# Kernel tuning notes

Measured on AMD Instinct MI355X. Metric: run time of the kernel, lower is better.

Reference implementation:

```python
import jax, jax.numpy as jnp
import numpy as np

L, B, T, S, W, H = 4, 2, 2048, 512, 512, 8  # layers, batch, n_ctx, cond units, width, heads
CH = W // H


def _ln(x, g, b):
    m = x.mean(-1, keepdims=True)
    v = ((x - m) ** 2).mean(-1, keepdims=True)
    return (x - m) * jax.lax.rsqrt(v + 1e-5) * g + b


def setup_inputs() -> dict:
    key = jax.random.key(0)
    ks = jax.random.split(key, 16)
    std = 0.25 * np.sqrt(1.0 / W)  # init_scale * sqrt(1/width), as in Transformer.__init__
    f32 = jnp.float32
    d = {
        "x": jax.random.normal(ks[0], (B, T, W), f32),
        "cond_k": jax.random.normal(ks[1], (B, S, W), f32),
        "cond_v": jax.random.normal(ks[2], (B, S, W), f32),
        # stacked per-layer params; weights stored [in, out] (torch Linear transposed)
        "qkv_w": jax.random.normal(ks[3], (L, W, 3 * W), f32) * std,
        "qkv_b": jnp.zeros((L, 3 * W), f32),
        "attn_proj_w": jax.random.normal(ks[4], (L, W, W), f32) * std,
        "attn_proj_b": jnp.zeros((L, W), f32),
        "cross_proj_w": jax.random.normal(ks[5], (L, W, W), f32) * std,
        "cross_proj_b": jnp.zeros((L, W), f32),
        "fc_w": jax.random.normal(ks[6], (L, W, 4 * W), f32) * std,
        "fc_b": jnp.zeros((L, 4 * W), f32),
        "mlp_proj_w": jax.random.normal(ks[7], (L, 4 * W, W), f32) * std,
        "mlp_proj_b": jnp.zeros((L, W), f32),
        "ln1_g": jnp.ones((L, W), f32), "ln1_b": jnp.zeros((L, W), f32),
        "ln3_g": jnp.ones((L, W), f32), "ln3_b": jnp.zeros((L, W), f32),
        "ln4_g": jnp.ones((L, W), f32), "ln4_b": jnp.zeros((L, W), f32),
    }
    return d


def reference(x, cond_k, cond_v, qkv_w, qkv_b, attn_proj_w, attn_proj_b,
              cross_proj_w, cross_proj_b, fc_w, fc_b, mlp_proj_w, mlp_proj_b,
              ln1_g, ln1_b, ln3_g, ln3_b, ln4_g, ln4_b):
    b, t, w = x.shape
    ch = w // H
    scale = 1.0 / np.sqrt(np.sqrt(ch))  # applied to both q and k, as in torch code
    kk = cond_k.reshape(b, -1, H, ch)
    vv = cond_v.reshape(b, -1, H, ch)
    n_layers = qkv_w.shape[0]
    for i in range(n_layers):
        # ---- self-attention ----
        h = _ln(x, ln1_g[i], ln1_b[i])
        qkv = (h @ qkv_w[i] + qkv_b[i]).reshape(b, t, H, 3 * ch)
        q, k, v = qkv[..., :ch], qkv[..., ch:2 * ch], qkv[..., 2 * ch:]
        wts = jnp.einsum('bthc,bshc->bhts', q * scale, k * scale)
        wts = jax.nn.softmax(wts.astype(jnp.float32), axis=-1).astype(wts.dtype)
        a = jnp.einsum('bhts,bshc->bthc', wts, v).reshape(b, t, w)
        x = x + a @ attn_proj_w[i] + attn_proj_b[i]
        # ---- cross-attention (q is ln_3(x) directly, no q projection) ----
        h = _ln(x, ln3_g[i], ln3_b[i])
        q = h.reshape(b, t, H, ch)
        wts = jnp.einsum('bthc,bshc->bhts', q * scale, kk * scale)
        wts = jax.nn.softmax(wts.astype(jnp.float32), axis=-1).astype(wts.dtype)
        a = jnp.einsum('bhts,bshc->bthc', wts, vv).reshape(b, t, w)
        x = x + a @ cross_proj_w[i] + cross_proj_b[i]
        # ---- MLP (exact erf GELU, as torch nn.GELU default) ----
        h = _ln(x, ln4_g[i], ln4_b[i])
        h = jax.nn.gelu(h @ fc_w[i] + fc_b[i], approximate=False)
        x = x + h @ mlp_proj_w[i] + mlp_proj_b[i]
    return x
```

## Files before the change

kernel.cpp:

```cpp
#include <hip/hip_runtime.h>
#include <hip/hip_bf16.h>
#include <cstdint>


typedef __bf16 bf16;
typedef __bf16 bf16x8 __attribute__((ext_vector_type(8)));
typedef float f32x4 __attribute__((ext_vector_type(4)));

#define AS1(p) ((__attribute__((address_space(1))) void*)(uintptr_t)(p))
#define AS3(p) ((__attribute__((address_space(3))) void*)(p))

__device__ __forceinline__ unsigned short bf2us(bf16 v) {
    return __builtin_bit_cast(unsigned short, v);
}

__global__ __launch_bounds__(256) void ln_kernel(const float* __restrict__ x,
                                                 const float* __restrict__ gam,
                                                 const float* __restrict__ bet,
                                                 bf16* __restrict__ h) {
    int row  = blockIdx.x * 4 + (threadIdx.x >> 6);
    int lane = threadIdx.x & 63;
    const float4* xr = (const float4*)(x + (size_t)row * 512) + lane * 2;
    float4 a = xr[0], b = xr[1];
    float s  = a.x + a.y + a.z + a.w + b.x + b.y + b.z + b.w;
    float ss = a.x * a.x + a.y * a.y + a.z * a.z + a.w * a.w +
               b.x * b.x + b.y * b.y + b.z * b.z + b.w * b.w;
#pragma unroll
    for (int off = 1; off < 64; off <<= 1) {
        s  += __shfl_xor(s, off);
        ss += __shfl_xor(ss, off);
    }
    float mean = s * (1.f / 512.f);
    float var  = ss * (1.f / 512.f) - mean * mean;
    float rstd = rsqrtf(fmaxf(var, 0.f) + 1e-5f);
    const float4* gr = (const float4*)gam + lane * 2;
    const float4* br = (const float4*)bet + lane * 2;
    float4 g0 = gr[0], g1 = gr[1], b0 = br[0], b1 = br[1];
    bf16x8 hv;
    hv[0] = (bf16)((a.x - mean) * rstd * g0.x + b0.x);
    hv[1] = (bf16)((a.y - mean) * rstd * g0.y + b0.y);
    hv[2] = (bf16)((a.z - mean) * rstd * g0.z + b0.z);
    hv[3] = (bf16)((a.w - mean) * rstd * g0.w + b0.w);
    hv[4] = (bf16)((b.x - mean) * rstd * g1.x + b1.x);
    hv[5] = (bf16)((b.y - mean) * rstd * g1.y + b1.y);
    hv[6] = (bf16)((b.z - mean) * rstd * g1.z + b1.z);
    hv[7] = (bf16)((b.w - mean) * rstd * g1.w + b1.w);
    *(bf16x8*)(h + (size_t)row * 512 + lane * 8) = hv;
}

__global__ void wtrans_kernel(const float* __restrict__ in, bf16* __restrict__ out,
                              int K, int N) {
    __shared__ float tile[32][33];
    int n0 = blockIdx.x * 32, k0 = blockIdx.y * 32;
    const float* ip = in + (size_t)blockIdx.z * K * N;
    bf16* op = out + (size_t)blockIdx.z * N * K;
#pragma unroll
    for (int i = threadIdx.y; i < 32; i += 8)
        tile[i][threadIdx.x] = ip[(size_t)(k0 + i) * N + n0 + threadIdx.x];
    __syncthreads();
#pragma unroll
    for (int i = threadIdx.y; i < 32; i += 8)
        op[(size_t)(n0 + i) * K + k0 + threadIdx.x] = (bf16)tile[threadIdx.x][i];
}

__global__ void cvt_kernel(const float* __restrict__ in, bf16* __restrict__ out, int n) {
    int i = (blockIdx.x * 256 + threadIdx.x) * 8;
    if (i + 8 <= n) {
        const float4* p = (const float4*)(in + i);
        float4 a = p[0], b = p[1];
        bf16x8 v;
        v[0] = (bf16)a.x; v[1] = (bf16)a.y; v[2] = (bf16)a.z; v[3] = (bf16)a.w;
        v[4] = (bf16)b.x; v[5] = (bf16)b.y; v[6] = (bf16)b.z; v[7] = (bf16)b.w;
        *(bf16x8*)(out + i) = v;
    }
}

__global__ __launch_bounds__(256) void vtrans_self(const bf16* __restrict__ qkvb,
                                                   bf16* __restrict__ VTs, int T_) {
    __shared__ bf16 tl[64][66];
    int tb = blockIdx.x * 64;
    int bh = blockIdx.y;
    int b = bh >> 3, h = bh & 7;
    int tid = threadIdx.x;
#pragma unroll
    for (int e = 0; e < 2; ++e) {
        int idx = e * 256 + tid;
        int t = idx >> 3, ci = (idx & 7) * 8;
        bf16x8 v = *(const bf16x8*)(qkvb + ((size_t)b * T_ + tb + t) * 1536 +
                                    h * 192 + 128 + ci);
#pragma unroll
        for (int j = 0; j < 8; ++j) tl[ci + j][t] = v[j];
    }
    __syncthreads();
#pragma unroll
    for (int e = 0; e < 2; ++e) {
        int idx = e * 256 + tid;
        int ch = idx >> 3, ti = (idx & 7) * 8;
        bf16x8 v;
#pragma unroll
        for (int j = 0; j < 8; ++j) v[j] = tl[ch][ti + j];
        *(bf16x8*)(VTs + ((size_t)bh * 64 + ch) * T_ + tb + ti) = v;
    }
}

__global__ __launch_bounds__(256) void vtrans_cross(const float* __restrict__ cv,
                                                    bf16* __restrict__ VTc, int S_) {
    __shared__ bf16 tl[64][66];
    int sb = blockIdx.x * 64;
    int bh = blockIdx.y;
    int b = bh >> 3, h = bh & 7;
    int tid = threadIdx.x;
#pragma unroll
    for (int e = 0; e < 4; ++e) {
        int idx = e * 256 + tid;
        int s = idx >> 4, ci = (idx & 15) * 4;
        float4 v = *(const float4*)(cv + ((size_t)b * S_ + sb + s) * 512 + h * 64 + ci);
        tl[ci + 0][s] = (bf16)v.x; tl[ci + 1][s] = (bf16)v.y;
        tl[ci + 2][s] = (bf16)v.z; tl[ci + 3][s] = (bf16)v.w;
    }
    __syncthreads();
#pragma unroll
    for (int e = 0; e < 2; ++e) {
        int idx = e * 256 + tid;
        int ch = idx >> 3, si = (idx & 7) * 8;
        bf16x8 v;
#pragma unroll
        for (int j = 0; j < 8; ++j) v[j] = tl[ch][si + j];
        *(bf16x8*)(VTc + ((size_t)bh * 64 + ch) * S_ + sb + si) = v;
    }
}

template <int EPI, int BM>
__global__ __launch_bounds__(256) void gemm_kernel(const bf16* __restrict__ A,
                                                   const bf16* __restrict__ Bt,
                                                   const float* __restrict__ bias,
                                                   const float* res, void* out,
                                                   int M, int N, int K) {
    constexpr int MI = (BM + 31) / 32;
    __shared__ __align__(16) bf16 As[BM * 64];
    __shared__ __align__(16) bf16 Bs[128 * 64];
    int tiles_n = N >> 7;
    int bid = blockIdx.x;
    int cpx = gridDim.x >> 3;
    bid = (bid & 7) * cpx + (bid >> 3);
    int bm = bid / tiles_n, bn = bid % tiles_n;
    int tid = threadIdx.x, wave = tid >> 6, lane = tid & 63;
    int wm = wave >> 1, wn = wave & 1;
    int g = lane >> 4, cc = lane & 15;
    f32x4 acc[MI][4] = {};
    const bf16* Ag = A + (size_t)(bm * BM) * K;
    const bf16* Bg = Bt + (size_t)(bn << 7) * K;
    int scol = (tid & 7) * 8;

    for (int k0 = 0; k0 < K; k0 += 64) {
        __syncthreads();
#pragma unroll
        for (int e = 0; e < BM / 32; ++e) {
            int row = (e * 256 + tid) >> 3;
            __builtin_amdgcn_global_load_lds(AS1(Ag + (size_t)row * K + k0 + scol),
                                             AS3((char*)As + e * 4096 + wave * 1024), 16, 0, 0);
        }
#pragma unroll
        for (int e = 0; e < 4; ++e) {
            int row = (e * 256 + tid) >> 3;
            __builtin_amdgcn_global_load_lds(AS1(Bg + (size_t)row * K + k0 + scol),
                                             AS3((char*)Bs + e * 4096 + wave * 1024), 16, 0, 0);
        }
        __syncthreads();
#pragma unroll
        for (int kk = 0; kk < 2; ++kk) {
            bf16x8 af[MI], bfr[4];
#pragma unroll
            for (int mi = 0; mi < MI; ++mi)
                af[mi] = *(const bf16x8*)(As + (wm * (BM / 2) + mi * 16 + cc) * 64 + kk * 32 + g * 8);
#pragma unroll
            for (int ni = 0; ni < 4; ++ni)
                bfr[ni] = *(const bf16x8*)(Bs + (wn * 64 + ni * 16 + cc) * 64 + kk * 32 + g * 8);
#pragma unroll
            for (int mi = 0; mi < MI; ++mi)
#pragma unroll
                for (int ni = 0; ni < 4; ++ni)
                    acc[mi][ni] = __builtin_amdgcn_mfma_f32_16x16x32_bf16(
                        af[mi], bfr[ni], acc[mi][ni], 0, 0, 0);
        }
    }
    int m0 = bm * BM + wm * (BM / 2);
    int n0 = (bn << 7) + wn * 64;
#pragma unroll
    for (int ni = 0; ni < 4; ++ni) {
        int n = n0 + ni * 16 + cc;
        float bv = bias[n];
#pragma unroll
        for (int mi = 0; mi < MI; ++mi) {
#pragma unroll
            for (int r = 0; r < 4; ++r) {
                int m = m0 + mi * 16 + g * 4 + r;
                float v = acc[mi][ni][r] + bv;
                if (EPI == 1) v = 0.5f * v * (1.f + erff(v * 0.70710678118654752f));
                if (EPI == 2)
                    ((float*)out)[(size_t)m * N + n] = res[(size_t)m * N + n] + v;
                else
                    ((bf16*)out)[(size_t)m * N + n] = (bf16)v;
            }
        }
    }
}

__global__ __launch_bounds__(512) void attn_kernel(
    const bf16* __restrict__ Qp, int q_rs, int q_hs,
    const bf16* __restrict__ Kp, int k_rs, int k_hs,
    const bf16* __restrict__ Vt, int vt_s,
    bf16* __restrict__ Op, int T_, int S_) {
    __shared__ __align__(16) char SM[40960];

    int numQ = T_ >> 6;
    int phys = blockIdx.x;
    int cpx = gridDim.x >> 3;
    int bid = (phys & 7) * cpx + (phys >> 3);
    int qb = bid % numQ;
    int bh = bid / numQ;
    int b = bh >> 3, h = bh & 7;
    int tid = threadIdx.x, wave = tid >> 6, lane = tid & 63;
    int wq = wave >> 1, ws = wave & 1;
    int g = lane >> 4, cc = lane & 15;
    int qrow0 = qb * 64;
    int swz = (cc >> 1) & 3;

    const bf16* Qb = Qp + ((size_t)b * T_ + qrow0 + wq * 16) * q_rs + h * q_hs;
    const bf16* Kb = Kp + ((size_t)b * S_) * k_rs + h * k_hs;
    const bf16* Vtb = Vt + (size_t)bh * 64 * vt_s;

    const float QSC = 0.125f * 1.44269504088896f;
    bf16x8 qf[2];
#pragma unroll
    for (int kk = 0; kk < 2; ++kk) {
        bf16x8 raw = *(const bf16x8*)(Qb + (size_t)cc * q_rs + kk * 32 + g * 8);
        bf16x8 sc;
#pragma unroll
        for (int j = 0; j < 8; ++j) sc[j] = (bf16)((float)raw[j] * QSC);
        qf[kk] = sc;
    }

    float l_acc = 0.f;
    f32x4 o_acc[4] = {};
    char* Pw = SM + 32768 + wave * 1024;

    auto stage = [&](int s0, int buf) {
        int row = tid >> 3, cp = tid & 7;
        int col = (cp ^ (row & 7)) * 8;
        __builtin_amdgcn_global_load_lds(AS1(Kb + (size_t)(s0 + row) * k_rs + col),
                                         AS3(SM + buf * 8192 + wave * 1024), 16, 0, 0);
        __builtin_amdgcn_global_load_lds(AS1(Vtb + (size_t)row * vt_s + s0 + col),
                                         AS3(SM + 16384 + buf * 8192 + wave * 1024), 16, 0, 0);
    };

    stage(0, 0);
    __syncthreads();

    int nt = S_ >> 6;
    int cur = 0;
    for (int t = 0; t < nt; ++t) {
        if (t + 1 < nt) stage((t + 1) * 64, cur ^ 1);
        char* kbc = SM + cur * 8192;
        char* vbc = SM + 16384 + cur * 8192;
        f32x4 sf[2] = {};
        __builtin_amdgcn_s_setprio(1);
#pragma unroll
        for (int kk = 0; kk < 2; ++kk)
#pragma unroll
            for (int sn = 0; sn < 2; ++sn) {
                int row = ws * 32 + sn * 16 + cc;
                bf16x8 kf = *(const bf16x8*)(kbc + row * 128 + (((kk * 4 + g) ^ (cc & 7)) << 4));
                sf[sn] = __builtin_amdgcn_mfma_f32_16x16x32_bf16(kf, qf[kk], sf[sn], 0, 0, 0);
            }
        __builtin_amdgcn_s_setprio(0);
#pragma unroll
        for (int sn = 0; sn < 2; ++sn) {
            float p0 = exp2f(sf[sn][0]), p1 = exp2f(sf[sn][1]);
            float p2 = exp2f(sf[sn][2]), p3 = exp2f(sf[sn][3]);
            l_acc += (p0 + p1) + (p2 + p3);
            uint32_t u01 = (uint32_t)bf2us((bf16)p0) | ((uint32_t)bf2us((bf16)p1) << 16);
            uint32_t u23 = (uint32_t)bf2us((bf16)p2) | ((uint32_t)bf2us((bf16)p3) << 16);
            char* pb = Pw + cc * 64 + (((sn * 2 + (g >> 1)) ^ swz) << 4) + (g & 1) * 8;
            uint2 uu; uu.x = u01; uu.y = u23;
            *(uint2*)pb = uu;
        }
        __builtin_amdgcn_s_setprio(1);
        bf16x8 pa = *(const bf16x8*)(Pw + cc * 64 + ((g ^ swz) << 4));
#pragma unroll
        for (int ni = 0; ni < 4; ++ni) {
            int vrow = ni * 16 + cc;
            bf16x8 vf = *(const bf16x8*)(vbc + vrow * 128 + (((ws * 4 + g) ^ (cc & 7)) << 4));
            o_acc[ni] = __builtin_amdgcn_mfma_f32_16x16x32_bf16(pa, vf, o_acc[ni], 0, 0, 0);
        }
        __builtin_amdgcn_s_setprio(0);
        __syncthreads();
        cur ^= 1;
    }

    l_acc += __shfl_xor(l_acc, 16);
    l_acc += __shfl_xor(l_acc, 32);
    float* sco = (float*)SM;
    float* lf = (float*)(SM + 32768);
    float* scw = sco + wave * 1024;
#pragma unroll
    for (int ni = 0; ni < 4; ++ni)
#pragma unroll
        for (int r = 0; r < 4; ++r)
            scw[(4 * g + r) * 64 + ni * 16 + cc] = o_acc[ni][r];
    if (g == 0) lf[wave * 16 + cc] = l_acc;
    __syncthreads();
    int q = tid >> 3, c0 = (tid & 7) * 8;
    int wqq = q >> 4, qr = q & 15;
    float l = lf[(wqq * 2) * 16 + qr] + lf[(wqq * 2 + 1) * 16 + qr];
    float inv = 1.f / l;
    const float* p0p = sco + (wqq * 2) * 1024 + qr * 64 + c0;
    const float* p1p = sco + (wqq * 2 + 1) * 1024 + qr * 64 + c0;
    bf16x8 o1;
#pragma unroll
    for (int e = 0; e < 2; ++e) {
        float4 v0 = *(const float4*)(p0p + e * 4);
        float4 v1 = *(const float4*)(p1p + e * 4);
        o1[e * 4 + 0] = (bf16)((v0.x + v1.x) * inv);
        o1[e * 4 + 1] = (bf16)((v0.y + v1.y) * inv);
        o1[e * 4 + 2] = (bf16)((v0.z + v1.z) * inv);
        o1[e * 4 + 3] = (bf16)((v0.w + v1.w) * inv);
    }
    *(bf16x8*)(Op + ((size_t)b * T_ + qrow0 + q) * 512 + h * 64 + c0) = o1;
}

extern "C" void kernel_launch(void* const* d_in, const int* in_sizes, int n_in,
                              void* d_out, int out_size, void* d_ws, size_t ws_size,
                              hipStream_t stream) {
    const float* x_in    = (const float*)d_in[0];
    const float* cond_k  = (const float*)d_in[1];
    const float* cond_v  = (const float*)d_in[2];
    const float* qkv_w   = (const float*)d_in[3];
    const float* qkv_b   = (const float*)d_in[4];
    const float* attn_w  = (const float*)d_in[5];
    const float* attn_b  = (const float*)d_in[6];
    const float* cross_w = (const float*)d_in[7];
    const float* cross_b = (const float*)d_in[8];
    const float* fc_w    = (const float*)d_in[9];
    const float* fc_b    = (const float*)d_in[10];
    const float* mlp_w   = (const float*)d_in[11];
    const float* mlp_b   = (const float*)d_in[12];
    const float* ln1_g   = (const float*)d_in[13];
    const float* ln1_b   = (const float*)d_in[14];
    const float* ln3_g   = (const float*)d_in[15];
    const float* ln3_b   = (const float*)d_in[16];
    const float* ln4_g   = (const float*)d_in[17];
    const float* ln4_b   = (const float*)d_in[18];

    const int L = 4, T = 2048, S = 512, W = 512;
    const int M = 2 * T;

    char* ws = (char*)d_ws;
    size_t off = 0;
    auto carve = [&](size_t bytes) -> char* {
        char* p = ws + off;
        off += (bytes + 255) & ~(size_t)255;
        return p;
    };
    bf16* wqkv  = (bf16*)carve((size_t)L * 1536 * 512 * 2);
    bf16* wattn = (bf16*)carve((size_t)L * 512 * 512 * 2);
    bf16* wcrs  = (bf16*)carve((size_t)L * 512 * 512 * 2);
    bf16* wfc   = (bf16*)carve((size_t)L * 2048 * 512 * 2);
    bf16* wmlp  = (bf16*)carve((size_t)L * 512 * 2048 * 2);
    bf16* ckb   = (bf16*)carve((size_t)2 * S * W * 2);
    bf16* VTs   = (bf16*)carve((size_t)16 * 64 * T * 2);
    bf16* VTc   = (bf16*)carve((size_t)16 * 64 * S * 2);
    bf16* hbuf  = (bf16*)carve((size_t)M * 512 * 2);
    bf16* qkvb  = (bf16*)carve((size_t)M * 1536 * 2);
    bf16* abuf  = (bf16*)carve((size_t)M * 512 * 2);
    bf16* fcb   = (bf16*)carve((size_t)M * 2048 * 2);

    dim3 tb(32, 8);
    wtrans_kernel<<<dim3(1536 / 32, 512 / 32, L), tb, 0, stream>>>(qkv_w, wqkv, 512, 1536);
    wtrans_kernel<<<dim3(512 / 32, 512 / 32, L), tb, 0, stream>>>(attn_w, wattn, 512, 512);
    wtrans_kernel<<<dim3(512 / 32, 512 / 32, L), tb, 0, stream>>>(cross_w, wcrs, 512, 512);
    wtrans_kernel<<<dim3(2048 / 32, 512 / 32, L), tb, 0, stream>>>(fc_w, wfc, 512, 2048);
    wtrans_kernel<<<dim3(512 / 32, 2048 / 32, L), tb, 0, stream>>>(mlp_w, wmlp, 2048, 512);
    cvt_kernel<<<(2 * S * W) / 2048, 256, 0, stream>>>(cond_k, ckb, 2 * S * W);
    vtrans_cross<<<dim3(S / 64, 16), 256, 0, stream>>>(cond_v, VTc, S);

    float* x = (float*)d_out;
    hipMemcpyAsync(x, (const void*)x_in, (size_t)M * W * sizeof(float),
                   hipMemcpyDeviceToDevice, stream);

    const int nAttn = 16 * (T / 64);
    for (int i = 0; i < L; ++i) {
        ln_kernel<<<M / 4, 256, 0, stream>>>(x, ln1_g + i * 512, ln1_b + i * 512, hbuf);
        gemm_kernel<0, 64><<<(M / 64) * (1536 / 128), 256, 0, stream>>>(
            hbuf, wqkv + (size_t)i * 1536 * 512, qkv_b + i * 1536, nullptr, qkvb,
            M, 1536, 512);
        vtrans_self<<<dim3(T / 64, 16), 256, 0, stream>>>(qkvb, VTs, T);
        attn_kernel<<<nAttn, 512, 0, stream>>>(
            qkvb, 1536, 192, qkvb + 64, 1536, 192, VTs, T,
            abuf, T, T);
        gemm_kernel<2, 32><<<(M / 32) * (512 / 128), 256, 0, stream>>>(
            abuf, wattn + (size_t)i * 512 * 512, attn_b + i * 512, x, x,
            M, 512, 512);
        ln_kernel<<<M / 4, 256, 0, stream>>>(x, ln3_g + i * 512, ln3_b + i * 512, hbuf);
        attn_kernel<<<nAttn, 512, 0, stream>>>(
            hbuf, 512, 64, ckb, 512, 64, VTc, S,
            abuf, T, S);
        gemm_kernel<2, 32><<<(M / 32) * (512 / 128), 256, 0, stream>>>(
            abuf, wcrs + (size_t)i * 512 * 512, cross_b + i * 512, x, x,
            M, 512, 512);
        ln_kernel<<<M / 4, 256, 0, stream>>>(x, ln4_g + i * 512, ln4_b + i * 512, hbuf);
        gemm_kernel<1, 128><<<(M / 128) * (2048 / 128), 256, 0, stream>>>(
            hbuf, wfc + (size_t)i * 2048 * 512, fc_b + i * 2048, nullptr, fcb,
            M, 2048, 512);
        gemm_kernel<2, 32><<<(M / 32) * (512 / 128), 256, 0, stream>>>(
            fcb, wmlp + (size_t)i * 512 * 2048, mlp_b + i * 512, x, x,
            M, 512, 2048);
    }
}
```

Measured before the change: 654.5 us.

## Double-buffer GEMM LDS staging and fuse V transpose into QKV epilogue

The GEMM kernel now double-buffers its A/B shared-memory tiles, so the next K-slice is loaded while the current one feeds the MFMAs, and each iteration needs one barrier instead of two. The QKV GEMM gets a new epilogue mode that writes the V columns directly in transposed per-head layout, which removes the separate vtrans_self launch and its extra read and write of V. The cost is twice the LDS per block, which may lower occupancy, plus more complex epilogue indexing with the batch and T sizes hardcoded. V columns are still written only to the transposed buffer.

New measurement: 666.1 us. About the same (+1.8%).

```diff
diff --git a/kernel.cpp b/kernel.cpp
--- a/kernel.cpp
+++ b/kernel.cpp
@@ -75,34 +75,6 @@
     }
 }
 
-__global__ __launch_bounds__(256) void vtrans_self(const bf16* __restrict__ qkvb,
-                                                   bf16* __restrict__ VTs, int T_) {
-    __shared__ bf16 tl[64][66];
-    int tb = blockIdx.x * 64;
-    int bh = blockIdx.y;
-    int b = bh >> 3, h = bh & 7;
-    int tid = threadIdx.x;
-#pragma unroll
-    for (int e = 0; e < 2; ++e) {
-        int idx = e * 256 + tid;
-        int t = idx >> 3, ci = (idx & 7) * 8;
-        bf16x8 v = *(const bf16x8*)(qkvb + ((size_t)b * T_ + tb + t) * 1536 +
-                                    h * 192 + 128 + ci);
-#pragma unroll
-        for (int j = 0; j < 8; ++j) tl[ci + j][t] = v[j];
-    }
-    __syncthreads();
-#pragma unroll
-    for (int e = 0; e < 2; ++e) {
-        int idx = e * 256 + tid;
-        int ch = idx >> 3, ti = (idx & 7) * 8;
-        bf16x8 v;
-#pragma unroll
-        for (int j = 0; j < 8; ++j) v[j] = tl[ch][ti + j];
-        *(bf16x8*)(VTs + ((size_t)bh * 64 + ch) * T_ + tb + ti) = v;
-    }
-}
-
 __global__ __launch_bounds__(256) void vtrans_cross(const float* __restrict__ cv,
                                                     bf16* __restrict__ VTc, int S_) {
     __shared__ bf16 tl[64][66];
@@ -135,10 +107,12 @@
                                                    const bf16* __restrict__ Bt,
                                                    const float* __restrict__ bias,
                                                    const float* res, void* out,
-                                                   int M, int N, int K) {
-    constexpr int MI = (BM + 31) / 32;
-    __shared__ __align__(16) bf16 As[BM * 64];
-    __shared__ __align__(16) bf16 Bs[128 * 64];
+                                                   int M, int N, int K,
+                                                   bf16* __restrict__ vtout, int Tdim) {
+    constexpr int MI = BM / 32;
+    constexpr int ABYTES = BM * 128;
+    __shared__ __align__(16) bf16 As[2 * BM * 64];
+    __shared__ __align__(16) bf16 Bs[2 * 128 * 64];
     int tiles_n = N >> 7;
     int bid = blockIdx.x;
     int cpx = gridDim.x >> 3;
@@ -152,30 +126,40 @@
     const bf16* Bg = Bt + (size_t)(bn << 7) * K;
     int scol = (tid & 7) * 8;
 
-    for (int k0 = 0; k0 < K; k0 += 64) {
-        __syncthreads();
+    auto stage = [&](int k0, int buf) {
 #pragma unroll
         for (int e = 0; e < BM / 32; ++e) {
             int row = (e * 256 + tid) >> 3;
             __builtin_amdgcn_global_load_lds(AS1(Ag + (size_t)row * K + k0 + scol),
-                                             AS3((char*)As + e * 4096 + wave * 1024), 16, 0, 0);
+                                             AS3((char*)As + buf * ABYTES + e * 4096 + wave * 1024),
+                                             16, 0, 0);
         }
 #pragma unroll
         for (int e = 0; e < 4; ++e) {
             int row = (e * 256 + tid) >> 3;
             __builtin_amdgcn_global_load_lds(AS1(Bg + (size_t)row * K + k0 + scol),
-                                             AS3((char*)Bs + e * 4096 + wave * 1024), 16, 0, 0);
-        }
-        __syncthreads();
+                                             AS3((char*)Bs + buf * 16384 + e * 4096 + wave * 1024),
+                                             16, 0, 0);
+        }
+    };
+
+    stage(0, 0);
+    __syncthreads();
+    int nk = K >> 6;
+    int buf = 0;
+    for (int t = 0; t < nk; ++t) {
+        if (t + 1 < nk) stage((t + 1) * 64, buf ^ 1);
+        const bf16* Ab = As + buf * (BM * 64);
+        const bf16* Bb = Bs + buf * (128 * 64);
 #pragma unroll
         for (int kk = 0; kk < 2; ++kk) {
             bf16x8 af[MI], bfr[4];
 #pragma unroll
             for (int mi = 0; mi < MI; ++mi)
-                af[mi] = *(const bf16x8*)(As + (wm * (BM / 2) + mi * 16 + cc) * 64 + kk * 32 + g * 8);
+                af[mi] = *(const bf16x8*)(Ab + (wm * (BM / 2) + mi * 16 + cc) * 64 + kk * 32 + g * 8);
 #pragma unroll
             for (int ni = 0; ni < 4; ++ni)
-                bfr[ni] = *(const bf16x8*)(Bs + (wn * 64 + ni * 16 + cc) * 64 + kk * 32 + g * 8);
+                bfr[ni] = *(const bf16x8*)(Bb + (wn * 64 + ni * 16 + cc) * 64 + kk * 32 + g * 8);
 #pragma unroll
             for (int mi = 0; mi < MI; ++mi)
 #pragma unroll
@@ -183,24 +167,39 @@
                     acc[mi][ni] = __builtin_amdgcn_mfma_f32_16x16x32_bf16(
                         af[mi], bfr[ni], acc[mi][ni], 0, 0, 0);
         }
+        __syncthreads();
+        buf ^= 1;
     }
     int m0 = bm * BM + wm * (BM / 2);
     int n0 = (bn << 7) + wn * 64;
 #pragma unroll
     for (int ni = 0; ni < 4; ++ni) {
-        int n = n0 + ni * 16 + cc;
+        int nb = n0 + ni * 16;
+        int n = nb + cc;
         float bv = bias[n];
+        bool isv = (EPI == 3) && (((nb >> 6) % 3) == 2);
 #pragma unroll
         for (int mi = 0; mi < MI; ++mi) {
-#pragma unroll
-            for (int r = 0; r < 4; ++r) {
-                int m = m0 + mi * 16 + g * 4 + r;
-                float v = acc[mi][ni][r] + bv;
-                if (EPI == 1) v = 0.5f * v * (1.f + erff(v * 0.70710678118654752f));
-                if (EPI == 2)
-                    ((float*)out)[(size_t)m * N + n] = res[(size_t)m * N + n] + v;
-                else
-                    ((bf16*)out)[(size_t)m * N + n] = (bf16)v;
+            if (isv) {
+                int hh = n / 192, chn = (n % 192) - 128;
+                int mb = m0 + mi * 16 + g * 4;
+                int bb = mb >> 11, t = mb & 2047;
+                ushort4 pk;
+#pragma unroll
+                for (int r = 0; r < 4; ++r)
+                    ((unsigned short*)&pk)[r] = bf2us((bf16)(acc[mi][ni][r] + bv));
+                *(ushort4*)(vtout + ((size_t)(bb * 8 + hh) * 64 + chn) * Tdim + t) = pk;
+            } else {
+#pragma unroll
+                for (int r = 0; r < 4; ++r) {
+                    int m = m0 + mi * 16 + g * 4 + r;
+                    float v = acc[mi][ni][r] + bv;
+                    if (EPI == 1) v = 0.5f * v * (1.f + erff(v * 0.70710678118654752f));
+                    if (EPI == 2)
+                        ((float*)out)[(size_t)m * N + n] = res[(size_t)m * N + n] + v;
+                    else
+                        ((bf16*)out)[(size_t)m * N + n] = (bf16)v;
+                }
             }
         }
     }
@@ -391,29 +390,28 @@
     const int nAttn = 16 * (T / 64);
     for (int i = 0; i < L; ++i) {
         ln_kernel<<<M / 4, 256, 0, stream>>>(x, ln1_g + i * 512, ln1_b + i * 512, hbuf);
-        gemm_kernel<0, 64><<<(M / 64) * (1536 / 128), 256, 0, stream>>>(
+        gemm_kernel<3, 64><<<(M / 64) * (1536 / 128), 256, 0, stream>>>(
             hbuf, wqkv + (size_t)i * 1536 * 512, qkv_b + i * 1536, nullptr, qkvb,
-            M, 1536, 512);
-        vtrans_self<<<dim3(T / 64, 16), 256, 0, stream>>>(qkvb, VTs, T);
+            M, 1536, 512, VTs, T);
         attn_kernel<<<nAttn, 512, 0, stream>>>(
             qkvb, 1536, 192, qkvb + 64, 1536, 192, VTs, T,
             abuf, T, T);
         gemm_kernel<2, 32><<<(M / 32) * (512 / 128), 256, 0, stream>>>(
             abuf, wattn + (size_t)i * 512 * 512, attn_b + i * 512, x, x,
-            M, 512, 512);
+            M, 512, 512, nullptr, 0);
         ln_kernel<<<M / 4, 256, 0, stream>>>(x, ln3_g + i * 512, ln3_b + i * 512, hbuf);
         attn_kernel<<<nAttn, 512, 0, stream>>>(
             hbuf, 512, 64, ckb, 512, 64, VTc, S,
             abuf, T, S);
         gemm_kernel<2, 32><<<(M / 32) * (512 / 128), 256, 0, stream>>>(
             abuf, wcrs + (size_t)i * 512 * 512, cross_b + i * 512, x, x,
-            M, 512, 512);
+            M, 512, 512, nullptr, 0);
         ln_kernel<<<M / 4, 256, 0, stream>>>(x, ln4_g + i * 512, ln4_b + i * 512, hbuf);
         gemm_kernel<1, 128><<<(M / 128) * (2048 / 128), 256, 0, stream>>>(
             hbuf, wfc + (size_t)i * 2048 * 512, fc_b + i * 2048, nullptr, fcb,
-            M, 2048, 512);
+            M, 2048, 512, nullptr, 0);
         gemm_kernel<2, 32><<<(M / 32) * (512 / 128), 256, 0, stream>>>(
             fcb, wmlp + (size_t)i * 512 * 2048, mlp_b + i * 512, x, x,
-            M, 512, 2048);
-    }
-}
+            M, 512, 2048, nullptr, 0);
+    }
+}
```

## Double-buffer GEMM and attention tiles with vmcnt-counted barriers

Applied to the files above, without the earlier changes.

The GEMM kernel gets double-buffered LDS tiles and issues the next-but-one k-tile load right after computing the current one. The attention loop keeps two tiles in flight the same way. Barriers become explicit s_waitcnt vmcnt(N) plus s_barrier, so each wave waits only for the oldest outstanding loads rather than draining all memory traffic. The aim is to hide global-to-LDS latency behind MFMA work, at the cost of twice the GEMM LDS footprint (possibly lower occupancy) and reliance on exact vmcnt accounting, which breaks if the compiler emits other vector memory ops in the loop.

Result: faster. 639.0 us (-2.4%).

```diff
diff --git a/kernel.cpp b/kernel.cpp
--- a/kernel.cpp
+++ b/kernel.cpp
@@ -12,6 +12,20 @@
 
 __device__ __forceinline__ unsigned short bf2us(bf16 v) {
     return __builtin_bit_cast(unsigned short, v);
+}
+
+template <int N>
+__device__ __forceinline__ void vmbar() {
+    if constexpr (N == 0)      asm volatile("s_waitcnt vmcnt(0)\n\ts_barrier" ::: "memory");
+    else if constexpr (N == 2) asm volatile("s_waitcnt vmcnt(2)\n\ts_barrier" ::: "memory");
+    else if constexpr (N == 5) asm volatile("s_waitcnt vmcnt(5)\n\ts_barrier" ::: "memory");
+    else if constexpr (N == 6) asm volatile("s_waitcnt vmcnt(6)\n\ts_barrier" ::: "memory");
+    else if constexpr (N == 8) asm volatile("s_waitcnt vmcnt(8)\n\ts_barrier" ::: "memory");
+    __builtin_amdgcn_sched_barrier(0);
+}
+__device__ __forceinline__ void plainbar() {
+    asm volatile("s_barrier" ::: "memory");
+    __builtin_amdgcn_sched_barrier(0);
 }
 
 __global__ __launch_bounds__(256) void ln_kernel(const float* __restrict__ x,
@@ -136,9 +150,11 @@
                                                    const float* __restrict__ bias,
                                                    const float* res, void* out,
                                                    int M, int N, int K) {
-    constexpr int MI = (BM + 31) / 32;
-    __shared__ __align__(16) bf16 As[BM * 64];
-    __shared__ __align__(16) bf16 Bs[128 * 64];
+    constexpr int MI = BM / 32;
+    constexpr int LPW = BM / 32 + 4;
+    constexpr int ABYTES = BM * 128;
+    __shared__ __align__(16) bf16 As[2 * BM * 64];
+    __shared__ __align__(16) bf16 Bs[2 * 128 * 64];
     int tiles_n = N >> 7;
     int bid = blockIdx.x;
     int cpx = gridDim.x >> 3;
@@ -152,30 +168,39 @@
     const bf16* Bg = Bt + (size_t)(bn << 7) * K;
     int scol = (tid & 7) * 8;
 
-    for (int k0 = 0; k0 < K; k0 += 64) {
-        __syncthreads();
+    auto stage = [&](int k0, int buf) {
 #pragma unroll
         for (int e = 0; e < BM / 32; ++e) {
             int row = (e * 256 + tid) >> 3;
             __builtin_amdgcn_global_load_lds(AS1(Ag + (size_t)row * K + k0 + scol),
-                                             AS3((char*)As + e * 4096 + wave * 1024), 16, 0, 0);
+                                             AS3((char*)As + buf * ABYTES + e * 4096 + wave * 1024),
+                                             16, 0, 0);
         }
 #pragma unroll
         for (int e = 0; e < 4; ++e) {
             int row = (e * 256 + tid) >> 3;
             __builtin_amdgcn_global_load_lds(AS1(Bg + (size_t)row * K + k0 + scol),
-                                             AS3((char*)Bs + e * 4096 + wave * 1024), 16, 0, 0);
-        }
-        __syncthreads();
+                                             AS3((char*)Bs + buf * 16384 + e * 4096 + wave * 1024),
+                                             16, 0, 0);
+        }
+    };
+
+    int nk = K >> 6;
+    stage(0, 0);
+    stage(64, 1);
+    for (int t = 0; t < nk; ++t) {
+        if (t + 1 < nk) vmbar<LPW>(); else vmbar<0>();
+        const bf16* Ab = As + (t & 1) * (BM * 64);
+        const bf16* Bb = Bs + (t & 1) * (128 * 64);
 #pragma unroll
         for (int kk = 0; kk < 2; ++kk) {
             bf16x8 af[MI], bfr[4];
 #pragma unroll
             for (int mi = 0; mi < MI; ++mi)
-                af[mi] = *(const bf16x8*)(As + (wm * (BM / 2) + mi * 16 + cc) * 64 + kk * 32 + g * 8);
+                af[mi] = *(const bf16x8*)(Ab + (wm * (BM / 2) + mi * 16 + cc) * 64 + kk * 32 + g * 8);
 #pragma unroll
             for (int ni = 0; ni < 4; ++ni)
-                bfr[ni] = *(const bf16x8*)(Bs + (wn * 64 + ni * 16 + cc) * 64 + kk * 32 + g * 8);
+                bfr[ni] = *(const bf16x8*)(Bb + (wn * 64 + ni * 16 + cc) * 64 + kk * 32 + g * 8);
 #pragma unroll
             for (int mi = 0; mi < MI; ++mi)
 #pragma unroll
@@ -183,6 +208,8 @@
                     acc[mi][ni] = __builtin_amdgcn_mfma_f32_16x16x32_bf16(
                         af[mi], bfr[ni], acc[mi][ni], 0, 0, 0);
         }
+        plainbar();
+        if (t + 2 < nk) stage((t + 2) * 64, t & 1);
     }
     int m0 = bm * BM + wm * (BM / 2);
     int n0 = (bn << 7) + wn * 64;
@@ -254,15 +281,13 @@
                                          AS3(SM + 16384 + buf * 8192 + wave * 1024), 16, 0, 0);
     };
 
+    int nt = S_ >> 6;
     stage(0, 0);
-    __syncthreads();
-
-    int nt = S_ >> 6;
-    int cur = 0;
+    stage(64, 1);
     for (int t = 0; t < nt; ++t) {
-        if (t + 1 < nt) stage((t + 1) * 64, cur ^ 1);
-        char* kbc = SM + cur * 8192;
-        char* vbc = SM + 16384 + cur * 8192;
+        if (t + 1 < nt) vmbar<2>(); else vmbar<0>();
+        char* kbc = SM + (t & 1) * 8192;
+        char* vbc = SM + 16384 + (t & 1) * 8192;
         f32x4 sf[2] = {};
         __builtin_amdgcn_s_setprio(1);
 #pragma unroll
@@ -294,8 +319,8 @@
             o_acc[ni] = __builtin_amdgcn_mfma_f32_16x16x32_bf16(pa, vf, o_acc[ni], 0, 0, 0);
         }
         __builtin_amdgcn_s_setprio(0);
-        __syncthreads();
-        cur ^= 1;
+        plainbar();
+        if (t + 2 < nt) stage((t + 2) * 64, t & 1);
     }
 
     l_acc += __shfl_xor(l_acc, 16);
```
